# Optimization experiments

Measured on AMD Instinct MI355X. Metric: run time of the kernel, lower is better.

The kernel has to match this reference:

```python
import jax, jax.numpy as jnp
import numpy as np

B, R, N, D, H, QK, K = 32, 200, 200, 128, 8, 16, 10
CLIP = 10.0  # standard POMO logit clipping


def setup_inputs() -> dict:
    key = jax.random.key(0)
    ks = jax.random.split(key, 12)
    encoded_nodes = jax.random.normal(ks[0], (B, N, D), jnp.float32)
    distance = jax.random.uniform(ks[1], (B, N, N), jnp.float32)
    current = jax.random.randint(ks[2], (B, R), 0, N)
    u = jax.random.uniform(ks[3], (B, R, N))
    ninf_mask = jnp.where(u < 0.3, -jnp.inf, 0.0).astype(jnp.float32)
    s = 0.02
    Wq = jax.random.normal(ks[4], (2 * D, H * QK), jnp.float32) * s
    Wk = jax.random.normal(ks[5], (D, H * QK), jnp.float32) * s
    Wv = jax.random.normal(ks[6], (D, H * QK), jnp.float32) * s
    Wmhc = jax.random.normal(ks[7], (H * QK, D), jnp.float32) * s
    b_mhc = jnp.zeros((D,), jnp.float32)
    W1 = jax.random.normal(ks[8], (K * D, 5 * D), jnp.float32) * s
    b1 = jnp.zeros((5 * D,), jnp.float32)
    W2 = jax.random.normal(ks[9], (5 * D, D), jnp.float32) * s
    b2 = jnp.zeros((D,), jnp.float32)
    return {"encoded_nodes": encoded_nodes, "distance": distance, "ninf_mask": ninf_mask,
            "current": current, "Wq": Wq, "Wk": Wk, "Wv": Wv, "Wmhc": Wmhc, "b_mhc": b_mhc,
            "W1": W1, "b1": b1, "W2": W2, "b2": b2}


def _search_unvisited(current, distance, ninf_mask):
    # rows of distance at current nodes: [B,R,N] (avoids B*R*N*N materialization)
    dist_f = jnp.take_along_axis(distance, current[:, :, None], axis=1)
    dist_m = jnp.where(jnp.isfinite(ninf_mask), dist_f, jnp.inf)
    neg_vals, idx = jax.lax.top_k(-dist_m, K)  # k smallest distances
    vals = -neg_vals
    return jnp.where(jnp.isinf(vals), N, idx)  # pad index N for masked-out slots


def _gather_pad0(encoded_nodes, idx):
    padded = jnp.concatenate([encoded_nodes, jnp.zeros((B, 1, D), encoded_nodes.dtype)], axis=1)
    g = jnp.take_along_axis(padded, idx.reshape(B, R * K)[:, :, None], axis=1)
    return g.reshape(B, R, K, D)


def _gather_pad_avg(a):
    # replace all-zero (pad) rows by the mean of non-zero rows within each [K,D] group
    is_zero = jnp.sum(a, axis=-1) == 0  # [B,R,K]
    cnt = jnp.maximum(jnp.sum(~is_zero, axis=-1).astype(a.dtype), 1e-9)  # [B,R]
    mean = jnp.sum(a, axis=2) / cnt[..., None]  # [B,R,D]
    return jnp.where(is_zero[..., None], mean[:, :, None, :], a)


def reference(encoded_nodes, distance, ninf_mask, current,
              Wq, Wk, Wv, Wmhc, b_mhc, W1, b1, W2, b2):
    knn = _search_unvisited(current, distance, ninf_mask)         # [B,R,K]
    a = _gather_pad0(encoded_nodes, knn)                          # [B,R,K,D]
    b = _gather_pad_avg(a)                                        # [B,R,K,D]
    h = jnp.maximum(b.reshape(B, R, K * D) @ W1 + b1, 0.0)
    unv = h @ W2 + b2                                             # [B,R,D]
    cur_emb = jnp.take_along_axis(encoded_nodes, current[:, :, None], axis=1)  # [B,R,D]
    qin = jnp.concatenate([cur_emb, unv], axis=-1)                # [B,R,2D]
    q = (qin @ Wq).reshape(B, R, H, QK).transpose(0, 2, 1, 3)     # [B,H,R,QK]
    k = (encoded_nodes @ Wk).reshape(B, N, H, QK).transpose(0, 2, 1, 3)
    v = (encoded_nodes @ Wv).reshape(B, N, H, QK).transpose(0, 2, 1, 3)
    score = jnp.einsum('bhrd,bhnd->bhrn', q, k) / jnp.sqrt(jnp.float32(QK))
    score = score + ninf_mask[:, None]                            # [B,H,R,N]
    w = jax.nn.softmax(score, axis=-1)
    out = jnp.einsum('bhrn,bhnd->bhrd', w, v)
    out = out.transpose(0, 2, 1, 3).reshape(B, R, H * QK)
    mh = out @ Wmhc + b_mhc                                       # [B,R,D]
    sh = jnp.einsum('brd,bnd->brn', mh, encoded_nodes) / jnp.sqrt(jnp.float32(D))
    logits = CLIP * jnp.tanh(sh) + ninf_mask
    return jax.nn.softmax(logits, axis=-1)                        # [B,R,N]
```

## Files before the change

### kernel.cpp

```cpp
#include <hip/hip_runtime.h>
#include <hip/hip_bf16.h>
#include <math.h>

#define Bc 32
#define Rc 200
#define Nc 200
#define Dc 128
#define Hc 8
#define QKc 16
#define Kc 10
#define BRc (Bc*Rc)

typedef __attribute__((ext_vector_type(8))) short short8;
typedef __attribute__((ext_vector_type(4))) float f32x4;
typedef unsigned long long u64;

#define GLOAD_LDS16(g, l) __builtin_amdgcn_global_load_lds( \
    (const __attribute__((address_space(1))) void*)(g), \
    (__attribute__((address_space(3))) void*)(l), 16, 0, 0)

__device__ inline void transpose_tile(const float* __restrict__ src, int lds_,
                                      __hip_bfloat16* __restrict__ dst, int ldd,
                                      int k0, int n0, float scale)
{
    __shared__ float tile[32][33];
    int tx = threadIdx.x & 31, ty = threadIdx.x >> 5;
    #pragma unroll
    for (int i = ty; i < 32; i += 8)
        tile[i][tx] = src[(size_t)(k0 + i) * lds_ + n0 + tx];
    __syncthreads();
    #pragma unroll
    for (int i = ty; i < 32; i += 8)
        dst[(size_t)(n0 + i) * ldd + k0 + tx] = __float2bfloat16(tile[tx][i] * scale);
}

__global__ __launch_bounds__(256) void prep_knn_kernel(
    const float* __restrict__ W1, const float* __restrict__ W2,
    const float* __restrict__ Wq, const float* __restrict__ Wmhc,
    const float* __restrict__ Wk, const float* __restrict__ Wv,
    const float* __restrict__ b2, const float* __restrict__ enc,
    const float* __restrict__ dist, const float* __restrict__ mask,
    const int* __restrict__ cur,
    __hip_bfloat16* __restrict__ W1t, __hip_bfloat16* __restrict__ Wkvt,
    __hip_bfloat16* __restrict__ Wmb, __hip_bfloat16* __restrict__ Wcat,
    float* __restrict__ bq, __hip_bfloat16* __restrict__ encb,
    unsigned* __restrict__ aoff, __hip_bfloat16* __restrict__ hq,
    u64* __restrict__ maskbits)
{
    int bid = blockIdx.x;
    int t = threadIdx.x;
    if (bid < 800) {
        transpose_tile(W1, 640, W1t, 1280, (bid % 40) * 32, (bid / 40) * 32, 1.f);
    } else if (bid < 816) {
        int id = bid - 800;
        transpose_tile(Wk, 128, Wkvt, 128, (id & 3) * 32, (id >> 2) * 32, 1.f);
    } else if (bid < 832) {
        int id = bid - 816;
        transpose_tile(Wv, 128, Wkvt + 128 * 128, 128, (id & 3) * 32, (id >> 2) * 32, 1.f);
    } else if (bid < 848) {
        int e = (bid - 832) * 1024 + t * 4;
        #pragma unroll
        for (int j = 0; j < 4; ++j) Wmb[e + j] = __float2bfloat16(Wmhc[e + j]);
    } else if (bid < 864) {
        int id = bid - 848;
        transpose_tile(Wq, 128, Wcat, 768, (id & 3) * 32, (id >> 2) * 32, 0.25f);
    } else if (bid < 904) {
        int j0 = (bid - 864) * 16;
        int n = t & 127, half = t >> 7;
        #pragma unroll
        for (int jj = 0; jj < 8; ++jj) {
            int j = j0 + half * 8 + jj;
            float acc = 0.f;
            for (int k = 0; k < 128; ++k)
                acc = fmaf(W2[(size_t)j * 128 + k], Wq[(size_t)(128 + k) * 128 + n], acc);
            Wcat[(size_t)n * 768 + 128 + j] = __float2bfloat16(acc * 0.25f);
        }
    } else if (bid < 929) {
        size_t base = (size_t)(bid - 904) * 32768 + (size_t)t * 4;
        #pragma unroll 4
        for (int it = 0; it < 32; ++it) {
            size_t i = base + (size_t)it * 1024;
            float4 v = *(const float4*)(enc + i);
            encb[i + 0] = __float2bfloat16(v.x);
            encb[i + 1] = __float2bfloat16(v.y);
            encb[i + 2] = __float2bfloat16(v.z);
            encb[i + 3] = __float2bfloat16(v.w);
        }
    } else if (bid == 929) {
        if (t < 128) {
            float acc = 0.f;
            for (int k = 0; k < 128; ++k)
                acc = fmaf(b2[k], Wq[(size_t)(128 + k) * 128 + t], acc);
            bq[t] = acc * 0.25f;
        }
    } else {
        int lane = t & 63, w = t >> 6;
        int br = (bid - 930) * 4 + w;
        int b = br / Rc;
        int c = cur[br];
        const float* drow = dist + ((size_t)b * Nc + c) * Nc;
        const float* mrow = mask + (size_t)br * Nc;

        float v[4];
        #pragma unroll
        for (int j = 0; j < 4; ++j) {
            int n = lane + 64 * j;
            bool allowed = false;
            float val = INFINITY;
            if (n < Nc) {
                float mv = mrow[n];
                if (!isinf(mv)) { val = drow[n]; allowed = true; }
            }
            v[j] = val;
            u64 wb = __ballot(allowed);
            if (lane == 0) maskbits[(size_t)br * 4 + j] = wb;
        }
        int idxs[Kc];
        unsigned myrow = 0;
        #pragma unroll
        for (int k = 0; k < Kc; ++k) {
            float bv = v[0]; int bn = lane;
            #pragma unroll
            for (int j = 1; j < 4; ++j) {
                if (v[j] < bv) { bv = v[j]; bn = lane + 64 * j; }
            }
            #pragma unroll
            for (int off = 32; off > 0; off >>= 1) {
                float ov = __shfl_xor(bv, off);
                int   on = __shfl_xor(bn, off);
                if (ov < bv || (ov == bv && on < bn)) { bv = ov; bn = on; }
            }
            bool pad = isinf(bv);
            idxs[k] = pad ? Nc : bn;
            if (lane == k) myrow = pad ? (unsigned)(Bc * Nc + br) : (unsigned)(b * Nc + bn);
            int oj = bn >> 6, ol = bn & 63;
            if (!pad && lane == ol) v[oj] = INFINITY;
        }
        if (lane < Kc) aoff[(size_t)br * 16 + lane] = myrow << 7;

        const float* erow = enc + ((size_t)b * Nc + c) * Dc;
        __hip_bfloat16* hrow = hq + (size_t)br * 768;
        hrow[lane]      = __float2bfloat16(erow[lane]);
        hrow[lane + 64] = __float2bfloat16(erow[lane + 64]);

        if (idxs[Kc - 1] == Nc) {
            float cnt = 0.f;
            #pragma unroll
            for (int k = 0; k < Kc; ++k) cnt += (idxs[k] < Nc) ? 1.f : 0.f;
            float icnt = 1.f / fmaxf(cnt, 1e-9f);
            #pragma unroll
            for (int half = 0; half < 2; ++half) {
                int d = lane + 64 * half;
                float sum = 0.f;
                #pragma unroll
                for (int k = 0; k < Kc; ++k) {
                    if (idxs[k] < Nc)
                        sum += enc[((size_t)b * Nc + idxs[k]) * Dc + d];
                }
                encb[((size_t)(Bc * Nc) + br) * Dc + d] = __float2bfloat16(sum * icnt);
            }
        }
    }
}

__global__ __launch_bounds__(256) void fused_gemms_kernel(
    const __hip_bfloat16* __restrict__ encb, const unsigned* __restrict__ aoff,
    const __hip_bfloat16* __restrict__ W1t, const float* __restrict__ b1,
    const __hip_bfloat16* __restrict__ Wkvt, const __hip_bfloat16* __restrict__ Wmb,
    const float* __restrict__ bmhc, const float* __restrict__ enc,
    __hip_bfloat16* __restrict__ hq, __hip_bfloat16* __restrict__ kvf,
    __hip_bfloat16* __restrict__ em, float* __restrict__ be)
{
    __shared__ short Asl[2][64 * 32];
    __shared__ short Bsl[2][64 * 32];
    int bid = blockIdx.x;
    int tid = threadIdx.x;
    int wave = tid >> 6, lane = tid & 63;
    int lrow = lane >> 2;
    int cg   = lane & 3;
    int ss   = (lane >> 3) & 3;
    int gq   = (cg - ss) & 3;
    int wm = wave >> 1, wn = wave & 1;
    int rrow = lane & 15, quad = lane >> 4;
    int srd  = (rrow >> 1) & 3;
    int strip = (wave & 1) * 32;

    if (bid < 1000) {
        int m0 = (bid / 10) * 64, n0 = (bid % 10) * 64;
        unsigned o0[Kc], o1[Kc];
        if (wave < 2) {
            const unsigned* ap0 = aoff + (size_t)(m0 + strip + lrow) * 16;
            const unsigned* ap1 = ap0 + 16 * 16;
            #pragma unroll
            for (int j = 0; j < Kc; ++j) { o0[j] = ap0[j]; o1[j] = ap1[j]; }
        }
        const short* Eb = (const short*)encb;
        const short* gB0 = (const short*)W1t + (size_t)(n0 + strip + lrow) * 1280 + gq * 8;
        const short* gB1 = gB0 + (size_t)16 * 1280;

        f32x4 acc[2][2];
        #pragma unroll
        for (int i = 0; i < 2; ++i)
            #pragma unroll
            for (int j = 0; j < 2; ++j)
                acc[i][j] = (f32x4){0.f, 0.f, 0.f, 0.f};

        #pragma unroll
        for (int kt = 0; kt < 20; ++kt) {
            int k0 = kt * 64;
            int slot = kt >> 1;
            int dbase = (kt & 1) * 64 + gq * 8;
            __syncthreads();
            #pragma unroll
            for (int s = 0; s < 2; ++s) {
                if (wave < 2) {
                    GLOAD_LDS16(Eb + o0[slot] + dbase + s * 32, &Asl[s][strip * 32]);
                    GLOAD_LDS16(Eb + o1[slot] + dbase + s * 32, &Asl[s][(strip + 16) * 32]);
                } else {
                    GLOAD_LDS16(gB0 + k0 + s * 32, &Bsl[s][strip * 32]);
                    GLOAD_LDS16(gB1 + k0 + s * 32, &Bsl[s][(strip + 16) * 32]);
                }
            }
            __syncthreads();
            #pragma unroll
            for (int s = 0; s < 2; ++s) {
                short8 afr[2], bfr[2];
                #pragma unroll
                for (int mt = 0; mt < 2; ++mt)
                    afr[mt] = *(const short8*)&Asl[s][(wm * 32 + mt * 16 + rrow) * 32 + ((quad + srd) & 3) * 8];
                #pragma unroll
                for (int nt = 0; nt < 2; ++nt)
                    bfr[nt] = *(const short8*)&Bsl[s][(wn * 32 + nt * 16 + rrow) * 32 + ((quad + srd) & 3) * 8];
                #pragma unroll
                for (int mt = 0; mt < 2; ++mt)
                    #pragma unroll
                    for (int nt = 0; nt < 2; ++nt)
                        acc[mt][nt] = __builtin_amdgcn_mfma_f32_16x16x32_bf16(
                            afr[mt], bfr[nt], acc[mt][nt], 0, 0, 0);
            }
        }
        #pragma unroll
        for (int mt = 0; mt < 2; ++mt)
            #pragma unroll
            for (int nt = 0; nt < 2; ++nt) {
                int n = wn * 32 + nt * 16 + rrow;
                float bv = b1[n0 + n];
                #pragma unroll
                for (int i = 0; i < 4; ++i) {
                    int m = m0 + wm * 32 + mt * 16 + quad * 4 + i;
                    float vv = fmaxf(acc[mt][nt][i] + bv, 0.f);
                    hq[(size_t)m * 768 + 128 + n0 + n] = __float2bfloat16(vv);
                }
            }
    } else if (bid < 1600) {
        const short* Bbase; __hip_bfloat16* Cout; int ldc, m0, n0;
        if (bid < 1400) {
            int id = bid - 1000;
            Bbase = (const short*)Wkvt; Cout = kvf; ldc = 256;
            m0 = (id >> 2) * 64; n0 = (id & 3) * 64;
        } else {
            int id = bid - 1400;
            Bbase = (const short*)Wmb; Cout = em; ldc = 128;
            m0 = (id >> 1) * 64; n0 = (id & 1) * 64;
        }
        const short* g0 = (wave < 2)
            ? (const short*)encb + (size_t)(m0 + strip + lrow) * 128 + gq * 8
            : Bbase + (size_t)(n0 + strip + lrow) * 128 + gq * 8;
        const short* g1 = g0 + (size_t)16 * 128;

        f32x4 acc[2][2];
        #pragma unroll
        for (int i = 0; i < 2; ++i)
            #pragma unroll
            for (int j = 0; j < 2; ++j)
                acc[i][j] = (f32x4){0.f, 0.f, 0.f, 0.f};

        #pragma unroll
        for (int kt = 0; kt < 2; ++kt) {
            int k0 = kt * 64;
            __syncthreads();
            #pragma unroll
            for (int s = 0; s < 2; ++s) {
                short* l0 = (wave < 2) ? &Asl[s][strip * 32] : &Bsl[s][strip * 32];
                short* l1 = (wave < 2) ? &Asl[s][(strip + 16) * 32] : &Bsl[s][(strip + 16) * 32];
                GLOAD_LDS16(g0 + k0 + s * 32, l0);
                GLOAD_LDS16(g1 + k0 + s * 32, l1);
            }
            __syncthreads();
            #pragma unroll
            for (int s = 0; s < 2; ++s) {
                short8 afr[2], bfr[2];
                #pragma unroll
                for (int mt = 0; mt < 2; ++mt)
                    afr[mt] = *(const short8*)&Asl[s][(wm * 32 + mt * 16 + rrow) * 32 + ((quad + srd) & 3) * 8];
                #pragma unroll
                for (int nt = 0; nt < 2; ++nt)
                    bfr[nt] = *(const short8*)&Bsl[s][(wn * 32 + nt * 16 + rrow) * 32 + ((quad + srd) & 3) * 8];
                #pragma unroll
                for (int mt = 0; mt < 2; ++mt)
                    #pragma unroll
                    for (int nt = 0; nt < 2; ++nt)
                        acc[mt][nt] = __builtin_amdgcn_mfma_f32_16x16x32_bf16(
                            afr[mt], bfr[nt], acc[mt][nt], 0, 0, 0);
            }
        }
        #pragma unroll
        for (int mt = 0; mt < 2; ++mt)
            #pragma unroll
            for (int nt = 0; nt < 2; ++nt) {
                int n = wn * 32 + nt * 16 + rrow;
                #pragma unroll
                for (int i = 0; i < 4; ++i) {
                    int m = m0 + wm * 32 + mt * 16 + quad * 4 + i;
                    Cout[(size_t)m * ldc + n0 + n] = __float2bfloat16(acc[mt][nt][i]);
                }
            }
    } else {
        int i = (bid - 1600) * 256 + tid;
        if (i < Bc * Nc) {
            const float* row = enc + (size_t)i * 128;
            float acc = 0.f;
            #pragma unroll
            for (int dq = 0; dq < 32; ++dq) {
                float4 e4 = *(const float4*)(row + dq * 4);
                acc = fmaf(bmhc[dq * 4 + 0], e4.x, acc);
                acc = fmaf(bmhc[dq * 4 + 1], e4.y, acc);
                acc = fmaf(bmhc[dq * 4 + 2], e4.z, acc);
                acc = fmaf(bmhc[dq * 4 + 3], e4.w, acc);
            }
            be[i] = acc;
        }
    }
}

__global__ __launch_bounds__(256) void qgemm_kernel(
    const __hip_bfloat16* __restrict__ hq, const __hip_bfloat16* __restrict__ Wcat,
    const float* __restrict__ bq, __hip_bfloat16* __restrict__ q)
{
    __shared__ short Asl[2][64 * 32];
    __shared__ short Bsl[2][64 * 32];
    int tid = threadIdx.x;
    int wave = tid >> 6, lane = tid & 63;
    int m0 = blockIdx.y * 64, n0 = blockIdx.x * 64;
    int lrow = lane >> 2;
    int cg   = lane & 3;
    int ss   = (lane >> 3) & 3;
    int gq   = (cg - ss) & 3;
    int wm = wave >> 1, wn = wave & 1;
    int rrow = lane & 15, quad = lane >> 4;
    int srd  = (rrow >> 1) & 3;
    int strip = (wave & 1) * 32;

    const short* g0 = (wave < 2)
        ? (const short*)hq + (size_t)(m0 + strip + lrow) * 768 + gq * 8
        : (const short*)Wcat + (size_t)(n0 + strip + lrow) * 768 + gq * 8;
    const short* g1 = g0 + (size_t)16 * 768;

    f32x4 acc[2][2];
    #pragma unroll
    for (int i = 0; i < 2; ++i)
        #pragma unroll
        for (int j = 0; j < 2; ++j)
            acc[i][j] = (f32x4){0.f, 0.f, 0.f, 0.f};

    for (int k0 = 0; k0 < 768; k0 += 64) {
        __syncthreads();
        #pragma unroll
        for (int s = 0; s < 2; ++s) {
            short* l0 = (wave < 2) ? &Asl[s][strip * 32] : &Bsl[s][strip * 32];
            short* l1 = (wave < 2) ? &Asl[s][(strip + 16) * 32] : &Bsl[s][(strip + 16) * 32];
            GLOAD_LDS16(g0 + k0 + s * 32, l0);
            GLOAD_LDS16(g1 + k0 + s * 32, l1);
        }
        __syncthreads();
        #pragma unroll
        for (int s = 0; s < 2; ++s) {
            short8 afr[2], bfr[2];
            #pragma unroll
            for (int mt = 0; mt < 2; ++mt)
                afr[mt] = *(const short8*)&Asl[s][(wm * 32 + mt * 16 + rrow) * 32 + ((quad + srd) & 3) * 8];
            #pragma unroll
            for (int nt = 0; nt < 2; ++nt)
                bfr[nt] = *(const short8*)&Bsl[s][(wn * 32 + nt * 16 + rrow) * 32 + ((quad + srd) & 3) * 8];
            #pragma unroll
            for (int mt = 0; mt < 2; ++mt)
                #pragma unroll
                for (int nt = 0; nt < 2; ++nt)
                    acc[mt][nt] = __builtin_amdgcn_mfma_f32_16x16x32_bf16(
                        afr[mt], bfr[nt], acc[mt][nt], 0, 0, 0);
        }
    }

    #pragma unroll
    for (int mt = 0; mt < 2; ++mt) {
        #pragma unroll
        for (int nt = 0; nt < 2; ++nt) {
            int n = wn * 32 + nt * 16 + rrow;
            float bv = bq[n0 + n];
            #pragma unroll
            for (int i = 0; i < 4; ++i) {
                int m = m0 + wm * 32 + mt * 16 + quad * 4 + i;
                q[(size_t)m * 128 + n0 + n] = __float2bfloat16(acc[mt][nt][i] + bv);
            }
        }
    }
}

__global__ __launch_bounds__(256) void attn_mfma_kernel(
    const __hip_bfloat16* __restrict__ q, const __hip_bfloat16* __restrict__ kvf,
    const u64* __restrict__ maskbits, __hip_bfloat16* __restrict__ att)
{
    constexpr int RP = 208;
    constexpr int QS = 40;
    constexpr int VS = 232;
    __shared__ short Qs[RP * QS];
    __shared__ short Ks[RP * QS];
    __shared__ short Vt[16 * VS];
    __shared__ short Ps[4][16 * VS];
    __shared__ u64 smask[RP][4];

    int b = blockIdx.x >> 3, h = blockIdx.x & 7;
    int t = threadIdx.x;
    int wave = t >> 6, lane = t & 63;
    int rrow = lane & 15, quad = lane >> 4;

    const short8 z8 = {0, 0, 0, 0, 0, 0, 0, 0};
    for (int idx = t; idx < RP * 2; idx += 256) {
        int r = idx >> 1, g = idx & 1;
        short8 qa = z8, ka = z8;
        if (r < Rc) {
            qa = *(const short8*)((const short*)q + ((size_t)(b * Rc + r)) * 128 + h * 16 + g * 8);
            ka = *(const short8*)((const short*)kvf + ((size_t)(b * Nc + r)) * 256 + h * 16 + g * 8);
        }
        *(short8*)&Qs[r * QS + g * 8] = qa;
        *(short8*)&Ks[r * QS + g * 8] = ka;
        *(short8*)&Qs[r * QS + 16 + g * 8] = z8;
        *(short8*)&Ks[r * QS + 16 + g * 8] = z8;
    }
    if (t < Rc) {
        const short* vp = (const short*)kvf + ((size_t)(b * Nc + t)) * 256 + 128 + h * 16;
        short8 v0 = *(const short8*)vp;
        short8 v1 = *(const short8*)(vp + 8);
        #pragma unroll
        for (int d = 0; d < 8; ++d) Vt[d * VS + t] = v0[d];
        #pragma unroll
        for (int d = 0; d < 8; ++d) Vt[(d + 8) * VS + t] = v1[d];
    }
    for (int idx = t; idx < 16 * 32; idx += 256) {
        int d = idx >> 5, cN = 200 + (idx & 31);
        if (cN < VS) Vt[d * VS + cN] = 0;
    }
    for (int idx = lane; idx < 16 * 16; idx += 64) {
        int rr = idx >> 4, cc = 208 + (idx & 15);
        Ps[wave][rr * VS + cc] = 0;
    }
    for (int idx = t; idx < RP * 4; idx += 256) {
        int r = idx >> 2, w = idx & 3;
        smask[r][w] = (r < Rc) ? maskbits[((size_t)b * Rc + r) * 4 + w] : ~0ull;
    }
    __syncthreads();

    for (int rt = wave; rt < 13; rt += 4) {
        short8 qf = *(const short8*)&Qs[(rt * 16 + rrow) * QS + quad * 8];
        f32x4 sacc[13];
        #pragma unroll
        for (int nt = 0; nt < 13; ++nt) {
            short8 kf = *(const short8*)&Ks[(nt * 16 + rrow) * QS + quad * 8];
            sacc[nt] = __builtin_amdgcn_mfma_f32_16x16x32_bf16(
                qf, kf, (f32x4){0.f, 0.f, 0.f, 0.f}, 0, 0, 0);
        }
        float inv[4];
        #pragma unroll
        for (int i = 0; i < 4; ++i) {
            int r = rt * 16 + quad * 4 + i;
            u64 wv0 = smask[r][0], wv1 = smask[r][1], wv2 = smask[r][2], wv3 = smask[r][3];
            float mx = -INFINITY;
            #pragma unroll
            for (int nt = 0; nt < 13; ++nt) {
                u64 w = (nt < 4) ? wv0 : (nt < 8) ? wv1 : (nt < 12) ? wv2 : wv3;
                int sh = ((nt & 3) << 4) + rrow;
                float s = ((w >> sh) & 1ull) ? sacc[nt][i] : -INFINITY;
                sacc[nt][i] = s;
                mx = fmaxf(mx, s);
            }
            mx = fmaxf(mx, __shfl_xor(mx, 1));
            mx = fmaxf(mx, __shfl_xor(mx, 2));
            mx = fmaxf(mx, __shfl_xor(mx, 4));
            mx = fmaxf(mx, __shfl_xor(mx, 8));
            float l = 0.f;
            #pragma unroll
            for (int nt = 0; nt < 13; ++nt) {
                float p = __expf(sacc[nt][i] - mx);
                sacc[nt][i] = p;
                l += p;
            }
            l += __shfl_xor(l, 1);
            l += __shfl_xor(l, 2);
            l += __shfl_xor(l, 4);
            l += __shfl_xor(l, 8);
            inv[i] = (l > 0.f) ? 1.f / l : 0.f;
        }
        #pragma unroll
        for (int nt = 0; nt < 13; ++nt)
            #pragma unroll
            for (int i = 0; i < 4; ++i)
                *(__hip_bfloat16*)&Ps[wave][(quad * 4 + i) * VS + nt * 16 + rrow] =
                    __float2bfloat16(sacc[nt][i]);
        f32x4 oacc = (f32x4){0.f, 0.f, 0.f, 0.f};
        #pragma unroll
        for (int kt = 0; kt < 7; ++kt) {
            short8 pf = *(const short8*)&Ps[wave][rrow * VS + kt * 32 + quad * 8];
            short8 vf = *(const short8*)&Vt[rrow * VS + kt * 32 + quad * 8];
            oacc = __builtin_amdgcn_mfma_f32_16x16x32_bf16(pf, vf, oacc, 0, 0, 0);
        }
        #pragma unroll
        for (int i = 0; i < 4; ++i) {
            int r = rt * 16 + quad * 4 + i;
            if (r < Rc)
                att[((size_t)(b * Rc + r)) * 128 + h * 16 + rrow] =
                    __float2bfloat16(oacc[i] * inv[i]);
        }
    }
}

__global__ __launch_bounds__(256) void logits_mfma_kernel(
    const __hip_bfloat16* __restrict__ att, const __hip_bfloat16* __restrict__ em,
    const float* __restrict__ be, const u64* __restrict__ maskbits,
    float* __restrict__ out)
{
    __shared__ short Asl[128 * 32];
    __shared__ short Bsl[128 * 32];
    __shared__ u64 sm[128][4];
    __shared__ float sbe[128];
    int b = blockIdx.x;
    int m0 = blockIdx.y * 128;
    int n0 = blockIdx.z * 128;
    int tid = threadIdx.x;
    int wave = tid >> 6, lane = tid & 63;

    for (int idx = tid; idx < 512; idx += 256) {
        int r = idx >> 2, w = idx & 3;
        int gr = m0 + r;
        sm[r][w] = (gr < Rc) ? maskbits[((size_t)b * Rc + gr) * 4 + w] : 0ull;
    }
    if (tid < 128) {
        int gn = n0 + tid;
        sbe[tid] = (gn < Nc) ? be[(size_t)b * Nc + gn] : 0.f;
    }

    int lrow = lane >> 2;
    int cg   = lane & 3;
    int ss   = (lane >> 3) & 3;
    int gq   = (cg - ss) & 3;
    const short* Ab = (const short*)(att + (size_t)b * Rc * 128);
    const short* Bb = (const short*)(em + (size_t)b * Nc * 128);
    const short* gA0 = Ab + (size_t)(m0 + wave * 32 + lrow) * 128 + gq * 8;
    const short* gA1 = gA0 + (size_t)16 * 128;
    const short* gB0 = Bb + (size_t)(n0 + wave * 32 + lrow) * 128 + gq * 8;
    const short* gB1 = gB0 + (size_t)16 * 128;
    short* lA0 = &Asl[(wave * 32) * 32];
    short* lA1 = &Asl[(wave * 32 + 16) * 32];
    short* lB0 = &Bsl[(wave * 32) * 32];
    short* lB1 = &Bsl[(wave * 32 + 16) * 32];

    int wm = wave >> 1, wn = wave & 1;
    int rrow = lane & 15, quad = lane >> 4;
    int srd  = (rrow >> 1) & 3;

    f32x4 acc[4][4];
    #pragma unroll
    for (int i = 0; i < 4; ++i)
        #pragma unroll
        for (int j = 0; j < 4; ++j)
            acc[i][j] = (f32x4){0.f, 0.f, 0.f, 0.f};

    for (int k0 = 0; k0 < 128; k0 += 32) {
        __syncthreads();
        GLOAD_LDS16(gA0 + k0, lA0);
        GLOAD_LDS16(gA1 + k0, lA1);
        GLOAD_LDS16(gB0 + k0, lB0);
        GLOAD_LDS16(gB1 + k0, lB1);
        __syncthreads();
        short8 afr[4], bfr[4];
        #pragma unroll
        for (int mt = 0; mt < 4; ++mt) {
            int rowa = wm * 64 + mt * 16 + rrow;
            afr[mt] = *(const short8*)&Asl[rowa * 32 + ((quad + srd) & 3) * 8];
            int rowb = wn * 64 + mt * 16 + rrow;
            bfr[mt] = *(const short8*)&Bsl[rowb * 32 + ((quad + srd) & 3) * 8];
        }
        #pragma unroll
        for (int mt = 0; mt < 4; ++mt)
            #pragma unroll
            for (int nt = 0; nt < 4; ++nt)
                acc[mt][nt] = __builtin_amdgcn_mfma_f32_16x16x32_bf16(
                    afr[mt], bfr[nt], acc[mt][nt], 0, 0, 0);
    }

    const float scale = 0.08838834764831843f;
    #pragma unroll
    for (int mt = 0; mt < 4; ++mt) {
        #pragma unroll
        for (int nt = 0; nt < 4; ++nt) {
            int nl = wn * 64 + nt * 16 + rrow;
            int n = n0 + nl;
            #pragma unroll
            for (int i = 0; i < 4; ++i) {
                int r = m0 + wm * 64 + mt * 16 + quad * 4 + i;
                if (r < Rc && n < Nc) {
                    u64 w = sm[r - m0][n >> 6];
                    float sh = (acc[mt][nt][i] + sbe[nl]) * scale;
                    float lg = ((w >> (n & 63)) & 1ull)
                             ? 10.f * tanhf(sh) : -INFINITY;
                    out[((size_t)b * Rc + r) * Nc + n] = lg;
                }
            }
        }
    }
}

__global__ __launch_bounds__(64) void softmax_kernel(float* __restrict__ out)
{
    int br = blockIdx.x;
    float* row = out + (size_t)br * Nc;
    int t = threadIdx.x;
    float v[4]; float m = -INFINITY;
    #pragma unroll
    for (int j = 0; j < 4; ++j) {
        int n = t + 64 * j;
        v[j] = (n < Nc) ? row[n] : -INFINITY;
        m = fmaxf(m, v[j]);
    }
    #pragma unroll
    for (int off = 32; off > 0; off >>= 1) m = fmaxf(m, __shfl_xor(m, off));
    float e[4]; float s = 0.f;
    #pragma unroll
    for (int j = 0; j < 4; ++j) {
        e[j] = (v[j] == -INFINITY) ? 0.f : expf(v[j] - m);
        s += e[j];
    }
    #pragma unroll
    for (int off = 32; off > 0; off >>= 1) s += __shfl_xor(s, off);
    float inv = 1.f / s;
    #pragma unroll
    for (int j = 0; j < 4; ++j) {
        int n = t + 64 * j;
        if (n < Nc) row[n] = e[j] * inv;
    }
}

extern "C" void kernel_launch(void* const* d_in, const int* in_sizes, int n_in,
                              void* d_out, int out_size, void* d_ws, size_t ws_size,
                              hipStream_t stream)
{
    const float* enc  = (const float*)d_in[0];
    const float* dist = (const float*)d_in[1];
    const float* mask = (const float*)d_in[2];
    const int*   cur  = (const int*)d_in[3];
    const float* Wq   = (const float*)d_in[4];
    const float* Wk   = (const float*)d_in[5];
    const float* Wv   = (const float*)d_in[6];
    const float* Wmhc = (const float*)d_in[7];
    const float* bmhc = (const float*)d_in[8];
    const float* W1   = (const float*)d_in[9];
    const float* b1   = (const float*)d_in[10];
    const float* W2   = (const float*)d_in[11];
    const float* b2   = (const float*)d_in[12];
    float* out = (float*)d_out;

    char* ws = (char*)d_ws;
    size_t off = 0;
    auto alloc = [&](size_t bytes) { char* p = ws + off; off += (bytes + 255) & ~(size_t)255; return p; };
    __hip_bfloat16* W1t  = (__hip_bfloat16*)alloc((size_t)640 * 1280 * 2);
    __hip_bfloat16* Wkvt = (__hip_bfloat16*)alloc((size_t)256 * 128 * 2);
    __hip_bfloat16* Wmb  = (__hip_bfloat16*)alloc((size_t)128 * 128 * 2);
    __hip_bfloat16* Wcat = (__hip_bfloat16*)alloc((size_t)128 * 768 * 2);
    float* bq = (float*)alloc((size_t)128 * 4);
    __hip_bfloat16* encb = (__hip_bfloat16*)alloc((size_t)(Bc * Nc + BRc + 64) * Dc * 2);
    unsigned* aoff = (unsigned*)alloc((size_t)BRc * 16 * 4);
    __hip_bfloat16* hq   = (__hip_bfloat16*)alloc((size_t)BRc * 768 * 2);
    __hip_bfloat16* q    = (__hip_bfloat16*)alloc((size_t)BRc * 128 * 2);
    __hip_bfloat16* kvf  = (__hip_bfloat16*)alloc((size_t)Bc * Nc * 256 * 2);
    __hip_bfloat16* att  = (__hip_bfloat16*)alloc((size_t)(BRc + 64) * 128 * 2);
    __hip_bfloat16* em   = (__hip_bfloat16*)alloc((size_t)(Bc * Nc + 64) * 128 * 2);
    float* be = (float*)alloc((size_t)Bc * Nc * 4);
    u64* maskbits = (u64*)alloc((size_t)BRc * 4 * 8);

    prep_knn_kernel<<<2530, 256, 0, stream>>>(
        W1, W2, Wq, Wmhc, Wk, Wv, b2, enc, dist, mask, cur,
        W1t, Wkvt, Wmb, Wcat, bq, encb, aoff, hq, maskbits);
    fused_gemms_kernel<<<1625, 256, 0, stream>>>(
        encb, aoff, W1t, b1, Wkvt, Wmb, bmhc, enc, hq, kvf, em, be);
    qgemm_kernel<<<dim3(2, BRc / 64), 256, 0, stream>>>(hq, Wcat, bq, q);
    attn_mfma_kernel<<<Bc * Hc, 256, 0, stream>>>(q, kvf, maskbits, att);
    logits_mfma_kernel<<<dim3(Bc, 2, 2), 256, 0, stream>>>(att, em, be, maskbits, out);
    softmax_kernel<<<BRc, 64, 0, stream>>>(out);
}
```

Measured before the change: 185.8 us.

## Fuse logits GEMM with row softmax in a single full-row kernel

```diff
diff --git a/kernel.cpp b/kernel.cpp
--- a/kernel.cpp
+++ b/kernel.cpp
@@ -523,129 +523,99 @@
     }
 }
 
-__global__ __launch_bounds__(256) void logits_mfma_kernel(
+__global__ __launch_bounds__(256) void logits_softmax_kernel(
     const __hip_bfloat16* __restrict__ att, const __hip_bfloat16* __restrict__ em,
     const float* __restrict__ be, const u64* __restrict__ maskbits,
     float* __restrict__ out)
 {
-    __shared__ short Asl[128 * 32];
-    __shared__ short Bsl[128 * 32];
-    __shared__ u64 sm[128][4];
-    __shared__ float sbe[128];
-    int b = blockIdx.x;
-    int m0 = blockIdx.y * 128;
-    int n0 = blockIdx.z * 128;
-    int tid = threadIdx.x;
-    int wave = tid >> 6, lane = tid & 63;
-
-    for (int idx = tid; idx < 512; idx += 256) {
-        int r = idx >> 2, w = idx & 3;
-        int gr = m0 + r;
-        sm[r][w] = (gr < Rc) ? maskbits[((size_t)b * Rc + gr) * 4 + w] : 0ull;
-    }
-    if (tid < 128) {
-        int gn = n0 + tid;
-        sbe[tid] = (gn < Nc) ? be[(size_t)b * Nc + gn] : 0.f;
-    }
-
-    int lrow = lane >> 2;
-    int cg   = lane & 3;
-    int ss   = (lane >> 3) & 3;
-    int gq   = (cg - ss) & 3;
-    const short* Ab = (const short*)(att + (size_t)b * Rc * 128);
-    const short* Bb = (const short*)(em + (size_t)b * Nc * 128);
-    const short* gA0 = Ab + (size_t)(m0 + wave * 32 + lrow) * 128 + gq * 8;
-    const short* gA1 = gA0 + (size_t)16 * 128;
-    const short* gB0 = Bb + (size_t)(n0 + wave * 32 + lrow) * 128 + gq * 8;
-    const short* gB1 = gB0 + (size_t)16 * 128;
-    short* lA0 = &Asl[(wave * 32) * 32];
-    short* lA1 = &Asl[(wave * 32 + 16) * 32];
-    short* lB0 = &Bsl[(wave * 32) * 32];
-    short* lB1 = &Bsl[(wave * 32 + 16) * 32];
-
-    int wm = wave >> 1, wn = wave & 1;
-    int rrow = lane & 15, quad = lane >> 4;
-    int srd  = (rrow >> 1) & 3;
-
-    f32x4 acc[4][4];
-    #pragma unroll
-    for (int i = 0; i < 4; ++i)
-        #pragma unroll
-        for (int j = 0; j < 4; ++j)
-            acc[i][j] = (f32x4){0.f, 0.f, 0.f, 0.f};
-
-    for (int k0 = 0; k0 < 128; k0 += 32) {
-        __syncthreads();
-        GLOAD_LDS16(gA0 + k0, lA0);
-        GLOAD_LDS16(gA1 + k0, lA1);
-        GLOAD_LDS16(gB0 + k0, lB0);
-        GLOAD_LDS16(gB1 + k0, lB1);
-        __syncthreads();
-        short8 afr[4], bfr[4];
-        #pragma unroll
-        for (int mt = 0; mt < 4; ++mt) {
-            int rowa = wm * 64 + mt * 16 + rrow;
-            afr[mt] = *(const short8*)&Asl[rowa * 32 + ((quad + srd) & 3) * 8];
-            int rowb = wn * 64 + mt * 16 + rrow;
-            bfr[mt] = *(const short8*)&Bsl[rowb * 32 + ((quad + srd) & 3) * 8];
-        }
-        #pragma unroll
-        for (int mt = 0; mt < 4; ++mt)
-            #pragma unroll
-            for (int nt = 0; nt < 4; ++nt)
-                acc[mt][nt] = __builtin_amdgcn_mfma_f32_16x16x32_bf16(
-                    afr[mt], bfr[nt], acc[mt][nt], 0, 0, 0);
-    }
+    __shared__ short Asl[4][64 * 32];
+    __shared__ short Bsl[4][208 * 32];
+    __shared__ u64 sm[64][4];
+    __shared__ float sbe[208];
+    int b = blockIdx.x, m0 = blockIdx.y * 64;
+    int t = threadIdx.x, wave = t >> 6, lane = t & 63;
+    int lrow = lane >> 2, cg = lane & 3, ss = (lane >> 3) & 3, gq = (cg - ss) & 3;
+    int rrow = lane & 15, quad = lane >> 4, srd = (rrow >> 1) & 3;
+
+    const short* Aa = (const short*)att + ((size_t)b * Rc + m0) * 128;
+    const short* Ben = (const short*)em + (size_t)b * Nc * 128;
+
+    #pragma unroll
+    for (int kc = 0; kc < 4; ++kc)
+        GLOAD_LDS16(Aa + (size_t)(wave * 16 + lrow) * 128 + kc * 32 + gq * 8,
+                    &Asl[kc][(wave * 16) * 32]);
+    for (int cch = wave; cch < 13; cch += 4)
+        #pragma unroll
+        for (int kc = 0; kc < 4; ++kc)
+            GLOAD_LDS16(Ben + (size_t)(cch * 16 + lrow) * 128 + kc * 32 + gq * 8,
+                        &Bsl[kc][(cch * 16) * 32]);
+    {
+        int r = t >> 2, w = t & 3;
+        sm[r][w] = (m0 + r < Rc) ? maskbits[((size_t)b * Rc + m0 + r) * 4 + w] : 0ull;
+    }
+    if (t < 208) sbe[t] = (t < Nc) ? be[(size_t)b * Nc + t] : 0.f;
+    __syncthreads();
+
+    short8 afr[4];
+    #pragma unroll
+    for (int kc = 0; kc < 4; ++kc)
+        afr[kc] = *(const short8*)&Asl[kc][(wave * 16 + rrow) * 32 + ((quad + srd) & 3) * 8];
+
+    f32x4 acc[13];
+    #pragma unroll
+    for (int nt = 0; nt < 13; ++nt)
+        acc[nt] = (f32x4){0.f, 0.f, 0.f, 0.f};
+    #pragma unroll
+    for (int nt = 0; nt < 13; ++nt)
+        #pragma unroll
+        for (int kc = 0; kc < 4; ++kc) {
+            short8 bfr = *(const short8*)
+                &Bsl[kc][(nt * 16 + rrow) * 32 + ((quad + srd) & 3) * 8];
+            acc[nt] = __builtin_amdgcn_mfma_f32_16x16x32_bf16(afr[kc], bfr, acc[nt], 0, 0, 0);
+        }
 
     const float scale = 0.08838834764831843f;
     #pragma unroll
-    for (int mt = 0; mt < 4; ++mt) {
-        #pragma unroll
-        for (int nt = 0; nt < 4; ++nt) {
-            int nl = wn * 64 + nt * 16 + rrow;
-            int n = n0 + nl;
-            #pragma unroll
-            for (int i = 0; i < 4; ++i) {
-                int r = m0 + wm * 64 + mt * 16 + quad * 4 + i;
-                if (r < Rc && n < Nc) {
-                    u64 w = sm[r - m0][n >> 6];
-                    float sh = (acc[mt][nt][i] + sbe[nl]) * scale;
-                    float lg = ((w >> (n & 63)) & 1ull)
-                             ? 10.f * tanhf(sh) : -INFINITY;
-                    out[((size_t)b * Rc + r) * Nc + n] = lg;
-                }
-            }
-        }
-    }
-}
-
-__global__ __launch_bounds__(64) void softmax_kernel(float* __restrict__ out)
-{
-    int br = blockIdx.x;
-    float* row = out + (size_t)br * Nc;
-    int t = threadIdx.x;
-    float v[4]; float m = -INFINITY;
-    #pragma unroll
-    for (int j = 0; j < 4; ++j) {
-        int n = t + 64 * j;
-        v[j] = (n < Nc) ? row[n] : -INFINITY;
-        m = fmaxf(m, v[j]);
-    }
-    #pragma unroll
-    for (int off = 32; off > 0; off >>= 1) m = fmaxf(m, __shfl_xor(m, off));
-    float e[4]; float s = 0.f;
-    #pragma unroll
-    for (int j = 0; j < 4; ++j) {
-        e[j] = (v[j] == -INFINITY) ? 0.f : expf(v[j] - m);
-        s += e[j];
-    }
-    #pragma unroll
-    for (int off = 32; off > 0; off >>= 1) s += __shfl_xor(s, off);
-    float inv = 1.f / s;
-    #pragma unroll
-    for (int j = 0; j < 4; ++j) {
-        int n = t + 64 * j;
-        if (n < Nc) row[n] = e[j] * inv;
+    for (int i = 0; i < 4; ++i) {
+        int rloc = wave * 16 + quad * 4 + i;
+        int r = m0 + rloc;
+        u64 w0 = sm[rloc][0], w1 = sm[rloc][1], w2 = sm[rloc][2], w3 = sm[rloc][3];
+        float vals[13];
+        float mx = -INFINITY;
+        #pragma unroll
+        for (int nt = 0; nt < 13; ++nt) {
+            u64 w = (nt < 4) ? w0 : (nt < 8) ? w1 : (nt < 12) ? w2 : w3;
+            int sh = ((nt & 3) << 4) + rrow;
+            float lg = ((w >> sh) & 1ull)
+                     ? 10.f * tanhf((acc[nt][i] + sbe[nt * 16 + rrow]) * scale)
+                     : -INFINITY;
+            vals[nt] = lg;
+            mx = fmaxf(mx, lg);
+        }
+        mx = fmaxf(mx, __shfl_xor(mx, 1));
+        mx = fmaxf(mx, __shfl_xor(mx, 2));
+        mx = fmaxf(mx, __shfl_xor(mx, 4));
+        mx = fmaxf(mx, __shfl_xor(mx, 8));
+        float l = 0.f;
+        #pragma unroll
+        for (int nt = 0; nt < 13; ++nt) {
+            float p = (vals[nt] == -INFINITY) ? 0.f : __expf(vals[nt] - mx);
+            vals[nt] = p;
+            l += p;
+        }
+        l += __shfl_xor(l, 1);
+        l += __shfl_xor(l, 2);
+        l += __shfl_xor(l, 4);
+        l += __shfl_xor(l, 8);
+        float inv = (l > 0.f) ? 1.f / l : 0.f;
+        if (r < Rc) {
+            #pragma unroll
+            for (int nt = 0; nt < 13; ++nt) {
+                int n = nt * 16 + rrow;
+                if (n < Nc)
+                    out[((size_t)b * Rc + r) * Nc + n] = vals[nt] * inv;
+            }
+        }
     }
 }
 
@@ -693,6 +663,5 @@
         encb, aoff, W1t, b1, Wkvt, Wmb, bmhc, enc, hq, kvf, em, be);
     qgemm_kernel<<<dim3(2, BRc / 64), 256, 0, stream>>>(hq, Wcat, bq, q);
     attn_mfma_kernel<<<Bc * Hc, 256, 0, stream>>>(q, kvf, maskbits, att);
-    logits_mfma_kernel<<<dim3(Bc, 2, 2), 256, 0, stream>>>(att, em, be, maskbits, out);
-    softmax_kernel<<<BRc, 64, 0, stream>>>(out);
+    logits_softmax_kernel<<<dim3(Bc, 4), 256, 0, stream>>>(att, em, be, maskbits, out);
 }
```

New measurement: 177.8 us. -4.3%, faster.
